# Kernel optimization log

Hardware: AMD Instinct MI355X
Metric: run time of the kernel (lower is better)

Reference implementation:

```python
import jax, jax.numpy as jnp
import numpy as np

DT = 1.0  # time step (ms), plain constant in the source (not a Parameter)


def setup_inputs() -> dict:
    key = jax.random.key(0)
    N, T = 4096, 8192
    # scale randn currents so r_m * I/1000 ~ 20 mV -> realistic spiking
    I_input = jax.random.normal(key, (N, T), dtype=jnp.float32) * 200.0
    return {
        "I_input": I_input,
        "tau_m": jnp.float32(10.0),
        "v_th": jnp.float32(-55.0),
        "v_reset": jnp.float32(-75.0),
        "r_m": jnp.float32(100.0),
        "v_rest": jnp.float32(-70.0),
        "refractory": jnp.float32(2.0),
    }


def reference(I_input, tau_m, v_th, v_reset, r_m, v_rest, refractory):
    """LIF neuron scan, vectorized over N neurons. Per-neuron math matches
    LIFNeuron.simulate exactly: v[0]=v_rest, spikes[0]=0, then for t>=1
    either refractory clamp or Euler leak step with threshold/reset."""
    N, T = I_input.shape
    I_nA = I_input / 1000.0  # uA -> nA, as in the source

    def step(carry, I_prev):
        v_prev, refr = carry                      # each [N]
        in_refr = refr > 0
        dv = (v_rest - v_prev + r_m * I_prev) / tau_m * DT
        v_int = v_prev + dv
        spike = jnp.logical_and(jnp.logical_not(in_refr), v_int >= v_th)
        v_new = jnp.where(jnp.logical_or(in_refr, spike), v_reset, v_int)
        refr_new = jnp.where(in_refr, refr - 1.0,
                             jnp.where(spike, refractory / DT, refr))
        return (v_new, refr_new), spike.astype(jnp.float32)

    v0 = jnp.ones((N,), dtype=jnp.float32) * v_rest
    refr0 = jnp.zeros((N,), dtype=jnp.float32)
    # v[t] uses I[t-1]; scan over t = 1..T-1 -> feed I_nA[:, :T-1], time-major
    _, spikes_t = jax.lax.scan(step, (v0, refr0), jnp.transpose(I_nA[:, :-1]))
    spikes = jnp.concatenate(
        [jnp.zeros((N, 1), dtype=jnp.float32), jnp.transpose(spikes_t)], axis=1
    )  # [N, T]
    return spikes
```

## Files before the change

### kernel.cpp

```cpp
#include <hip/hip_runtime.h>


#define N_NEURONS 4096
#define T_STEPS   8192
#define BN        64
#define L_CHUNK   256
#define W_WARM    512
#define C_CHUNKS  (T_STEPS / L_CHUNK)
#define CN        (C_CHUNKS * N_NEURONS)

struct LifConst {
    float tau_m, v_th, v_rst, r_m, v_rest, a_rst, rcp_tau, rcp_1k;
    int   n_refr;
};

__device__ __forceinline__ float div_rn_fast(float a, float b, float rb) {
    const float q = __fmul_rn(a, rb);
    const float e = __fmaf_rn(-b, q, a);
    return __fmaf_rn(e, rb, q);
}

__device__ __forceinline__ LifConst load_consts(const float* p_tau,
        const float* p_vth, const float* p_vreset, const float* p_rm,
        const float* p_vrest, const float* p_refr) {
    LifConst K;
    K.tau_m = p_tau[0]; K.v_th = p_vth[0]; K.v_rst = p_vreset[0];
    K.r_m = p_rm[0];    K.v_rest = p_vrest[0];
    const float refr_set = __fdiv_rn(p_refr[0], 1.0f);
    K.n_refr  = (int)ceilf(refr_set);
    K.rcp_tau = __fdiv_rn(1.0f, K.tau_m);
    K.rcp_1k  = __fdiv_rn(1.0f, 1000.0f);
    K.a_rst   = __fsub_rn(K.v_rest, K.v_rst);
    return K;
}

__device__ __forceinline__ bool lif_step(const LifConst& K, float w, int t,
                                         float& v, float& a, int& refr_end) {
    const bool  inr   = t < refr_end;
    const float u     = __fadd_rn(a, w);
    const float dv    = div_rn_fast(u, K.tau_m, K.rcp_tau);
    const float vi    = __fadd_rn(v, dv);
    const bool  cross = vi >= K.v_th;
    const bool  rst   = inr || cross;
    const float a_ch  = __fsub_rn(K.v_rest, vi);
    v = rst ? K.v_rst : vi;
    a = rst ? K.a_rst : a_ch;
    const bool sp = (!inr) && cross;
    refr_end = sp ? (t + 1 + K.n_refr) : refr_end;
    return sp;
}

__device__ __forceinline__ void load_group(const float4* __restrict__ rowI4,
                                           int tb, float4 buf[8]) {
    #pragma unroll
    for (int j = 0; j < 8; ++j) buf[j] = rowI4[tb / 4 + j];
}

template <bool STORE>
__device__ __forceinline__ void sim_group32(const LifConst& K,
        const float4 buf[8], int tb, float4* __restrict__ rowO4,
        float& v, float& a, int& refr_end, float& prev) {
    #pragma unroll
    for (int j = 0; j < 8; ++j) {
        const float4 x  = buf[j];
        const int    c0 = tb + 4 * j;
        float4 s;
        s.x = prev;
        #pragma unroll
        for (int k = 0; k < 4; ++k) {
            const int t = c0 + k;
            float spf = 0.0f;
            if (t < T_STEPS - 1) {
                const float xi = (k == 0) ? x.x : (k == 1) ? x.y : (k == 2) ? x.z : x.w;
                const float w  = __fmul_rn(K.r_m, div_rn_fast(xi, 1000.0f, K.rcp_1k));
                const bool sp  = lif_step(K, w, t, v, a, refr_end);
                spf = sp ? 1.0f : 0.0f;
            }
            if      (k == 0) s.y = spf;
            else if (k == 1) s.z = spf;
            else if (k == 2) s.w = spf;
            else             prev = spf;
        }
        if (STORE) rowO4[c0 / 4] = s;
    }
}

__global__ __launch_bounds__(BN)
void lif_pass1(const float* __restrict__ I,
               const float* __restrict__ p_tau, const float* __restrict__ p_vth,
               const float* __restrict__ p_vreset, const float* __restrict__ p_rm,
               const float* __restrict__ p_vrest, const float* __restrict__ p_refr,
               float* __restrict__ out, float* __restrict__ ws)
{
    const int lane = threadIdx.x;
    const int c    = blockIdx.x & (C_CHUNKS - 1);
    const int nb   = blockIdx.x / C_CHUNKS;
    const int n    = nb * BN + lane;

    const LifConst K = load_consts(p_tau, p_vth, p_vreset, p_rm, p_vrest, p_refr);

    const float4* rowI4 = reinterpret_cast<const float4*>(I   + (size_t)n * T_STEPS);
    float4*       rowO4 = reinterpret_cast<float4*>      (out + (size_t)n * T_STEPS);

    const int tmain = c * L_CHUNK;
    const int t0    = (tmain >= W_WARM) ? (tmain - W_WARM) : 0;
    const int gmain = (tmain - t0) / 32;
    const int ngrp  = gmain + L_CHUNK / 32;

    float v, a, prev;
    int   refr_end;
    if (c == 0) {
        v = K.v_rest; a = __fsub_rn(K.v_rest, K.v_rest); refr_end = 0; prev = 0.0f;
    } else {
        v = K.v_rst;  a = K.a_rst;  refr_end = t0;  prev = 0.0f;
    }

    float* vS = ws + 0 * CN;  float* pS = ws + 1 * CN;
    int*   rS = (int*)(ws + 2 * CN);
    float* vE = ws + 3 * CN;  float* pE = ws + 4 * CN;
    int*   rE = (int*)(ws + 5 * CN);
    const int sidx = c * N_NEURONS + n;

    float4 bufA[8], bufB[8];
    load_group(rowI4, t0, bufA);

    for (int p = 0; p < gmain / 2; ++p) {
        const int gA = 2 * p, gB = 2 * p + 1;
        load_group(rowI4, t0 + gB * 32, bufB);
        sim_group32<false>(K, bufA, t0 + gA * 32, rowO4, v, a, refr_end, prev);
        load_group(rowI4, t0 + (gB + 1) * 32, bufA);
        sim_group32<false>(K, bufB, t0 + gB * 32, rowO4, v, a, refr_end, prev);
    }

    vS[sidx] = v; pS[sidx] = prev; rS[sidx] = refr_end;

    for (int p = 0; p < 4; ++p) {
        const int gA = gmain + 2 * p, gB = gA + 1;
        load_group(rowI4, t0 + gB * 32, bufB);
        sim_group32<true>(K, bufA, t0 + gA * 32, rowO4, v, a, refr_end, prev);
        if (gB + 1 < ngrp) load_group(rowI4, t0 + (gB + 1) * 32, bufA);
        sim_group32<true>(K, bufB, t0 + gB * 32, rowO4, v, a, refr_end, prev);
    }

    vE[sidx] = v; pE[sidx] = prev; rE[sidx] = refr_end;
}

__global__ __launch_bounds__(BN)
void lif_pass2(const float* __restrict__ I,
               const float* __restrict__ p_tau, const float* __restrict__ p_vth,
               const float* __restrict__ p_vreset, const float* __restrict__ p_rm,
               const float* __restrict__ p_vrest, const float* __restrict__ p_refr,
               float* __restrict__ out, const float* __restrict__ ws)
{
    const int n = blockIdx.x * BN + threadIdx.x;

    const LifConst K = load_consts(p_tau, p_vth, p_vreset, p_rm, p_vrest, p_refr);

    const float4* rowI4 = reinterpret_cast<const float4*>(I   + (size_t)n * T_STEPS);
    float4*       rowO4 = reinterpret_cast<float4*>      (out + (size_t)n * T_STEPS);

    const float* vS = ws + 0 * CN;  const float* pS = ws + 1 * CN;
    const int*   rS = (const int*)(ws + 2 * CN);
    const float* vE = ws + 3 * CN;  const float* pE = ws + 4 * CN;
    const int*   rE = (const int*)(ws + 5 * CN);

    float v        = vE[n];
    float prev     = pE[n];
    int   refr_end = rE[n];

    for (int c = 1; c < C_CHUNKS; ++c) {
        const int sidx  = c * N_NEURONS + n;
        const int tmain = c * L_CHUNK;

        const float vs = vS[sidx], ps = pS[sidx];
        const int   rs = rS[sidx];
        const float ve = vE[sidx], pe = pE[sidx];
        const int   re = rE[sidx];

        const bool refr_ok = (refr_end == rs) ||
                             ((refr_end <= tmain) && (rs <= tmain));
        const bool match   = (v == vs) && (prev == ps) && refr_ok;

        if (match) {
            v = ve; prev = pe; refr_end = re;
        } else {
            float a = __fsub_rn(K.v_rest, v);
            float4 bufA[8], bufB[8];
            load_group(rowI4, tmain, bufA);
            for (int p = 0; p < 4; ++p) {
                const int gA = 2 * p, gB = gA + 1;
                const int tA = tmain + gA * 32, tB = tmain + gB * 32;
                load_group(rowI4, tB, bufB);
                sim_group32<true>(K, bufA, tA, rowO4, v, a, refr_end, prev);
                if (gB + 1 < 8) load_group(rowI4, tmain + (gB + 1) * 32, bufA);
                sim_group32<true>(K, bufB, tB, rowO4, v, a, refr_end, prev);
            }
        }
    }
}

extern "C" void kernel_launch(void* const* d_in, const int* in_sizes, int n_in,
                              void* d_out, int out_size, void* d_ws, size_t ws_size,
                              hipStream_t stream)
{
    const float* I = (const float*)d_in[0];
    float* out = (float*)d_out;
    float* ws  = (float*)d_ws;

    lif_pass1<<<dim3((N_NEURONS / BN) * C_CHUNKS), dim3(BN), 0, stream>>>(
        I, (const float*)d_in[1], (const float*)d_in[2], (const float*)d_in[3],
        (const float*)d_in[4], (const float*)d_in[5], (const float*)d_in[6],
        out, ws);

    lif_pass2<<<dim3(N_NEURONS / BN), dim3(BN), 0, stream>>>(
        I, (const float*)d_in[1], (const float*)d_in[2], (const float*)d_in[3],
        (const float*)d_in[4], (const float*)d_in[5], (const float*)d_in[6],
        out, ws);
}
```

Baseline: 372.5 us.

## Remap pass-2 to one neuron per block with cooperative LDS staging

Result: slower. 384.1 us (+3.1%).

```diff
diff --git a/kernel.cpp b/kernel.cpp
--- a/kernel.cpp
+++ b/kernel.cpp
@@ -6,8 +6,9 @@
 #define BN        64
 #define L_CHUNK   256
 #define W_WARM    512
-#define C_CHUNKS  (T_STEPS / L_CHUNK)
+#define C_CHUNKS  32
 #define CN        (C_CHUNKS * N_NEURONS)
+#define NXCD      8
 
 struct LifConst {
     float tau_m, v_th, v_rst, r_m, v_rest, a_rst, rcp_tau, rcp_1k;
@@ -50,18 +51,19 @@
     return sp;
 }
 
-__device__ __forceinline__ void load_group(const float4* __restrict__ rowI4,
-                                           int tb, float4 buf[8]) {
+
+__device__ __forceinline__ void load_g64(const float4* __restrict__ rowI4,
+                                         int tb, float4 buf[16]) {
     #pragma unroll
-    for (int j = 0; j < 8; ++j) buf[j] = rowI4[tb / 4 + j];
+    for (int j = 0; j < 16; ++j) buf[j] = rowI4[tb / 4 + j];
 }
 
 template <bool STORE>
-__device__ __forceinline__ void sim_group32(const LifConst& K,
-        const float4 buf[8], int tb, float4* __restrict__ rowO4,
+__device__ __forceinline__ void sim_g64(const LifConst& K,
+        const float4 buf[16], int tb, float4* __restrict__ rowO4,
         float& v, float& a, int& refr_end, float& prev) {
     #pragma unroll
-    for (int j = 0; j < 8; ++j) {
+    for (int j = 0; j < 16; ++j) {
         const float4 x  = buf[j];
         const int    c0 = tb + 4 * j;
         float4 s;
@@ -85,7 +87,7 @@
     }
 }
 
-__global__ __launch_bounds__(BN)
+__global__ __launch_bounds__(BN, 2)
 void lif_pass1(const float* __restrict__ I,
                const float* __restrict__ p_tau, const float* __restrict__ p_vth,
                const float* __restrict__ p_vreset, const float* __restrict__ p_rm,
@@ -93,19 +95,21 @@
                float* __restrict__ out, float* __restrict__ ws)
 {
     const int lane = threadIdx.x;
-    const int c    = blockIdx.x & (C_CHUNKS - 1);
-    const int nb   = blockIdx.x / C_CHUNKS;
-    const int n    = nb * BN + lane;
+    const int r  = blockIdx.x % NXCD;
+    const int q  = blockIdx.x / NXCD;
+    const int c  = q % C_CHUNKS;
+    const int nb = r * (N_NEURONS / BN / NXCD) + q / C_CHUNKS;
+    const int n  = nb * BN + lane;
 
     const LifConst K = load_consts(p_tau, p_vth, p_vreset, p_rm, p_vrest, p_refr);
 
     const float4* rowI4 = reinterpret_cast<const float4*>(I   + (size_t)n * T_STEPS);
     float4*       rowO4 = reinterpret_cast<float4*>      (out + (size_t)n * T_STEPS);
 
-    const int tmain = c * L_CHUNK;
-    const int t0    = (tmain >= W_WARM) ? (tmain - W_WARM) : 0;
-    const int gmain = (tmain - t0) / 32;
-    const int ngrp  = gmain + L_CHUNK / 32;
+    const int tmain  = c * L_CHUNK;
+    const int t0     = (tmain >= W_WARM) ? (tmain - W_WARM) : 0;
+    const int warm64 = (tmain - t0) / 64;
+    const int ngrp64 = warm64 + L_CHUNK / 64;
 
     float v, a, prev;
     int   refr_end;
@@ -121,29 +125,30 @@
     int*   rE = (int*)(ws + 5 * CN);
     const int sidx = c * N_NEURONS + n;
 
-    float4 bufA[8], bufB[8];
-    load_group(rowI4, t0, bufA);
-
-    for (int p = 0; p < gmain / 2; ++p) {
+    float4 bufA[16], bufB[16];
+    load_g64(rowI4, t0, bufA);
+
+    for (int p = 0; p < warm64 / 2; ++p) {
         const int gA = 2 * p, gB = 2 * p + 1;
-        load_group(rowI4, t0 + gB * 32, bufB);
-        sim_group32<false>(K, bufA, t0 + gA * 32, rowO4, v, a, refr_end, prev);
-        load_group(rowI4, t0 + (gB + 1) * 32, bufA);
-        sim_group32<false>(K, bufB, t0 + gB * 32, rowO4, v, a, refr_end, prev);
+        load_g64(rowI4, t0 + gB * 64, bufB);
+        sim_g64<false>(K, bufA, t0 + gA * 64, rowO4, v, a, refr_end, prev);
+        load_g64(rowI4, t0 + (gB + 1) * 64, bufA);
+        sim_g64<false>(K, bufB, t0 + gB * 64, rowO4, v, a, refr_end, prev);
     }
 
     vS[sidx] = v; pS[sidx] = prev; rS[sidx] = refr_end;
 
-    for (int p = 0; p < 4; ++p) {
-        const int gA = gmain + 2 * p, gB = gA + 1;
-        load_group(rowI4, t0 + gB * 32, bufB);
-        sim_group32<true>(K, bufA, t0 + gA * 32, rowO4, v, a, refr_end, prev);
-        if (gB + 1 < ngrp) load_group(rowI4, t0 + (gB + 1) * 32, bufA);
-        sim_group32<true>(K, bufB, t0 + gB * 32, rowO4, v, a, refr_end, prev);
+    for (int p = 0; p < 2; ++p) {
+        const int gA = warm64 + 2 * p, gB = gA + 1;
+        load_g64(rowI4, t0 + gB * 64, bufB);
+        sim_g64<true>(K, bufA, t0 + gA * 64, rowO4, v, a, refr_end, prev);
+        if (gB + 1 < ngrp64) load_g64(rowI4, t0 + (gB + 1) * 64, bufA);
+        sim_g64<true>(K, bufB, t0 + gB * 64, rowO4, v, a, refr_end, prev);
     }
 
     vE[sidx] = v; pE[sidx] = prev; rE[sidx] = refr_end;
 }
+
 
 __global__ __launch_bounds__(BN)
 void lif_pass2(const float* __restrict__ I,
@@ -152,18 +157,21 @@
                const float* __restrict__ p_vrest, const float* __restrict__ p_refr,
                float* __restrict__ out, const float* __restrict__ ws)
 {
-    const int n = blockIdx.x * BN + threadIdx.x;
+    const int lane = threadIdx.x;
+    const int n    = blockIdx.x;
 
     const LifConst K = load_consts(p_tau, p_vth, p_vreset, p_rm, p_vrest, p_refr);
 
-    const float4* rowI4 = reinterpret_cast<const float4*>(I   + (size_t)n * T_STEPS);
-    float4*       rowO4 = reinterpret_cast<float4*>      (out + (size_t)n * T_STEPS);
+    const float4* rowI4 = reinterpret_cast<const float4*>(I + (size_t)n * T_STEPS);
+    float*        rowO  = out + (size_t)n * T_STEPS;
 
     const float* vS = ws + 0 * CN;  const float* pS = ws + 1 * CN;
     const int*   rS = (const int*)(ws + 2 * CN);
     const float* vE = ws + 3 * CN;  const float* pE = ws + 4 * CN;
     const int*   rE = (const int*)(ws + 5 * CN);
 
+    __shared__ float wsh[L_CHUNK];
+
     float v        = vE[n];
     float prev     = pE[n];
     int   refr_end = rE[n];
@@ -174,27 +182,68 @@
 
         const float vs = vS[sidx], ps = pS[sidx];
         const int   rs = rS[sidx];
-        const float ve = vE[sidx], pe = pE[sidx];
-        const int   re = rE[sidx];
 
         const bool refr_ok = (refr_end == rs) ||
                              ((refr_end <= tmain) && (rs <= tmain));
         const bool match   = (v == vs) && (prev == ps) && refr_ok;
 
         if (match) {
-            v = ve; prev = pe; refr_end = re;
+            v = vE[sidx]; prev = pE[sidx]; refr_end = rE[sidx];
         } else {
+            const float4 xi = rowI4[tmain / 4 + lane];
+            float4 wv;
+            wv.x = __fmul_rn(K.r_m, div_rn_fast(xi.x, 1000.0f, K.rcp_1k));
+            wv.y = __fmul_rn(K.r_m, div_rn_fast(xi.y, 1000.0f, K.rcp_1k));
+            wv.z = __fmul_rn(K.r_m, div_rn_fast(xi.z, 1000.0f, K.rcp_1k));
+            wv.w = __fmul_rn(K.r_m, div_rn_fast(xi.w, 1000.0f, K.rcp_1k));
+            *reinterpret_cast<float4*>(&wsh[4 * lane]) = wv;
+            __syncthreads();
+
             float a = __fsub_rn(K.v_rest, v);
-            float4 bufA[8], bufB[8];
-            load_group(rowI4, tmain, bufA);
-            for (int p = 0; p < 4; ++p) {
-                const int gA = 2 * p, gB = gA + 1;
-                const int tA = tmain + gA * 32, tB = tmain + gB * 32;
-                load_group(rowI4, tB, bufB);
-                sim_group32<true>(K, bufA, tA, rowO4, v, a, refr_end, prev);
-                if (gB + 1 < 8) load_group(rowI4, tmain + (gB + 1) * 32, bufA);
-                sim_group32<true>(K, bufB, tB, rowO4, v, a, refr_end, prev);
+            float sl0 = (lane == 0) ? prev : 0.0f;
+            float sl1 = 0.0f, sl2 = 0.0f, sl3 = 0.0f;
+
+            #define P2_SECTION(JJ, SLCUR, SEAM_STMT)                           \
+            {                                                                  \
+                float4 a0 = *reinterpret_cast<const float4*>(&wsh[64 * JJ]);   \
+                float4 a1 = *reinterpret_cast<const float4*>(&wsh[64 * JJ + 4]);\
+                for (int j2 = 0; j2 < 8; ++j2) {                               \
+                    float4 b0, b1;                                             \
+                    if (j2 < 7) {                                              \
+                        b0 = *reinterpret_cast<const float4*>(&wsh[64*JJ + 8*j2 + 8]); \
+                        b1 = *reinterpret_cast<const float4*>(&wsh[64*JJ + 8*j2 + 12]);\
+                    }                                                          \
+                    _Pragma("unroll")                                          \
+                    for (int m = 0; m < 8; ++m) {                              \
+                        const int t = tmain + 64 * JJ + 8 * j2 + m;            \
+                        float spf = 0.0f;                                      \
+                        if (t < T_STEPS - 1) {                                 \
+                            const float w = (m == 0) ? a0.x : (m == 1) ? a0.y  \
+                                          : (m == 2) ? a0.z : (m == 3) ? a0.w  \
+                                          : (m == 4) ? a1.x : (m == 5) ? a1.y  \
+                                          : (m == 6) ? a1.z : a1.w;            \
+                            const bool sp = lif_step(K, w, t, v, a, refr_end); \
+                            spf = sp ? 1.0f : 0.0f;                            \
+                        }                                                      \
+                        prev  = spf;                                           \
+                        SLCUR = (lane == 8 * j2 + m + 1) ? spf : SLCUR;        \
+                        if (m == 7) { SEAM_STMT }                              \
+                    }                                                          \
+                    if (j2 < 7) { a0 = b0; a1 = b1; }                          \
+                }                                                              \
             }
+
+            P2_SECTION(0, sl0, sl1 = (j2 == 7 && lane == 0) ? spf : sl1;)
+            P2_SECTION(1, sl1, sl2 = (j2 == 7 && lane == 0) ? spf : sl2;)
+            P2_SECTION(2, sl2, sl3 = (j2 == 7 && lane == 0) ? spf : sl3;)
+            P2_SECTION(3, sl3, )
+            #undef P2_SECTION
+
+            rowO[tmain +       lane] = sl0;
+            rowO[tmain +  64 + lane] = sl1;
+            rowO[tmain + 128 + lane] = sl2;
+            rowO[tmain + 192 + lane] = sl3;
+            __syncthreads();
         }
     }
 }
@@ -212,7 +261,7 @@
         (const float*)d_in[4], (const float*)d_in[5], (const float*)d_in[6],
         out, ws);
 
-    lif_pass2<<<dim3(N_NEURONS / BN), dim3(BN), 0, stream>>>(
+    lif_pass2<<<dim3(N_NEURONS), dim3(BN), 0, stream>>>(
         I, (const float*)d_in[1], (const float*)d_in[2], (const float*)d_in[3],
         (const float*)d_in[4], (const float*)d_in[5], (const float*)d_in[6],
         out, ws);
```
